# Performance work log

Hardware: AMD Instinct MI355X
Metric: run time of the kernel (lower is better)

Reference implementation:

```python
import jax, jax.numpy as jnp
from jax import lax
import numpy as np

B, S, D, H, O, V = 1024, 128, 256, 2048, 10, 10

def setup_inputs() -> dict:
    key = jax.random.key(0)
    ks = jax.random.split(key, 8)
    x = jax.random.randint(ks[0], (B, S), 0, V)
    embed = jax.random.normal(ks[1], (V, D), dtype=jnp.float32)
    sd_hx = 1.0 / np.sqrt(D)
    sd_hh = 1.0 / np.sqrt(H)
    W_hx = jax.random.uniform(ks[2], (H, D), minval=-sd_hx, maxval=sd_hx)
    b_hx = jax.random.uniform(ks[3], (H,), minval=-sd_hx, maxval=sd_hx)
    W_hh = jax.random.uniform(ks[4], (H, H), minval=-sd_hh, maxval=sd_hh)
    b_hh = jax.random.uniform(ks[5], (H,), minval=-sd_hh, maxval=sd_hh)
    W_oh = jax.random.uniform(ks[6], (O, H), minval=-sd_hh, maxval=sd_hh)
    b_oh = jax.random.uniform(ks[7], (O,), minval=-sd_hh, maxval=sd_hh)
    return {"x": x, "embed": embed, "W_hx": W_hx, "b_hx": b_hx,
            "W_hh": W_hh, "b_hh": b_hh, "W_oh": W_oh, "b_oh": b_oh}

def reference(x, embed, W_hx, b_hx, W_hh, b_hh, W_oh, b_oh):
    e = embed[x]                                   # [B,S,D]
    # precompute input-to-hidden projection for all steps (one big GEMM)
    xh = jnp.einsum('bsd,hd->bsh', e, W_hx) + b_hx  # [B,S,H]
    # step 0: torch code applies ONLY hx (no hh term, no hh bias)
    h0 = jnp.tanh(xh[:, 0])
    def step(h, xt):
        h = jnp.tanh(xt + h @ W_hh.T + b_hh)
        return h, None
    hT, _ = lax.scan(step, h0, jnp.swapaxes(xh[:, 1:], 0, 1))  # scan over time
    o = hT @ W_oh.T + b_oh                         # [B,O]
    return jax.nn.softmax(o, axis=1)               # nn.Softmax() on 2D -> dim=1
```

## Files before the change

kernel.cpp:

```cpp
#include <hip/hip_runtime.h>
#include <stdint.h>
#include <stddef.h>

#define B_ 1024
#define S_ 128
#define D_ 256
#define H_ 2048
#define O_ 10
#define V_ 10

#define BM 64
#define BN 64
#define BK 128
#define NKT (H_ / BK)

typedef unsigned short u16;
typedef short v8s __attribute__((ext_vector_type(8)));
typedef float v4f __attribute__((ext_vector_type(4)));
typedef u16 u16x4 __attribute__((ext_vector_type(4)));

__device__ __forceinline__ u16 f2bf(float f) {
  unsigned int u = __float_as_uint(f);
  u += 0x7FFFu + ((u >> 16) & 1u);
  return (u16)(u >> 16);
}
__device__ __forceinline__ float bf2f(u16 h) {
  return __uint_as_float(((unsigned int)h) << 16);
}
__device__ __forceinline__ float fast_tanh(float x) {
  float e = __expf(2.0f * x);
  return 1.0f - 2.0f / (e + 1.0f);
}
__device__ __forceinline__ void gl2lds16(const void* g, void* l) {
  __builtin_amdgcn_global_load_lds(
      (const __attribute__((address_space(1))) uint32_t*)g,
      (__attribute__((address_space(3))) uint32_t*)l, 16, 0, 0);
}

__global__ __launch_bounds__(256) void make_table(const float* __restrict__ embed,
                                                  const float* __restrict__ W_hx,
                                                  const float* __restrict__ b_hx,
                                                  float* __restrict__ Txh) {
  int idx = blockIdx.x * 256 + threadIdx.x;
  int v = idx >> 11, h = idx & 2047;
  const float4* e4 = (const float4*)(embed + v * D_);
  const float4* w4 = (const float4*)(W_hx + (size_t)h * D_);
  float s = b_hx[h];
#pragma unroll 4
  for (int d = 0; d < D_ / 4; ++d) {
    float4 a = e4[d], b = w4[d];
    s = fmaf(a.x, b.x, s); s = fmaf(a.y, b.y, s);
    s = fmaf(a.z, b.z, s); s = fmaf(a.w, b.w, s);
  }
  Txh[idx] = s;
}

__global__ __launch_bounds__(256) void conv_w(const float* __restrict__ W,
                                              u16* __restrict__ Wb) {
  int i = blockIdx.x * 256 + threadIdx.x;
  float4 w = ((const float4*)W)[i];
  u16x4 o = { f2bf(w.x), f2bf(w.y), f2bf(w.z), f2bf(w.w) };
  ((u16x4*)Wb)[i] = o;
}

__global__ __launch_bounds__(256) void init_h0(const float* __restrict__ Txh,
                                               const int* __restrict__ x,
                                               u16* __restrict__ H0) {
  int idx = blockIdx.x * 256 + threadIdx.x;
  int b = idx >> 11, j = idx & 2047;
  int xv = x[b * S_];
  H0[idx] = f2bf(fast_tanh(Txh[xv * H_ + j]));
}


__device__ __forceinline__ void stage_tiles(const u16* __restrict__ Hin,
                                            const u16* __restrict__ Wb,
                                            u16* __restrict__ As, u16* __restrict__ Bs,
                                            int bm, int bn, int kbase, int tid, int w) {
#pragma unroll
  for (int i = 0; i < 4; ++i) {
    int s = i * 256 + tid;
    int m = s >> 4;
    int cg = (s & 15) ^ (m & 15);
    const u16* g = Hin + (size_t)(bm + m) * H_ + kbase + cg * 8;
    u16* lp = As + (size_t)(i * 256 + (w << 6)) * 8;
    gl2lds16(g, lp);
  }
#pragma unroll
  for (int i = 0; i < 4; ++i) {
    int s = i * 256 + tid;
    int n = s >> 4;
    int cg = (s & 15) ^ (n & 15);
    const u16* g = Wb + (size_t)(bn + n) * H_ + kbase + cg * 8;
    u16* lp = Bs + (size_t)(i * 256 + (w << 6)) * 8;
    gl2lds16(g, lp);
  }
}

__global__ __launch_bounds__(256, 2) void rnn_step(const u16* __restrict__ Hin,
                                                   const u16* __restrict__ Wb,
                                                   const float* __restrict__ Txh,
                                                   const int* __restrict__ x,
                                                   const float* __restrict__ b_hh,
                                                   u16* __restrict__ Hout,
                                                   int t) {
  __shared__ __align__(16) u16 As[2][BM * BK];
  __shared__ __align__(16) u16 Bs[2][BN * BK];

  const int tid = threadIdx.x;
  const int bid = blockIdx.x;
  const int xcd = bid & 7;
  const int sl  = bid >> 3;
  const int xr = xcd >> 2, xc = xcd & 3;
  const int bm = (xr * 8 + (sl >> 3)) * BM;
  const int bn = (xc * 8 + (sl & 7)) * BN;

  const int w = tid >> 6, l = tid & 63;
  const int wr = w >> 1, wc = w & 1;
  const int lane16 = l & 15, quad = l >> 4;

  v4f acc[2][2];
#pragma unroll
  for (int i = 0; i < 2; ++i)
#pragma unroll
    for (int j = 0; j < 2; ++j) acc[i][j] = (v4f){0.f, 0.f, 0.f, 0.f};

  stage_tiles(Hin, Wb, As[0], Bs[0], bm, bn, 0, tid, w);
  __syncthreads();

  for (int kt = 0; kt < NKT; ++kt) {
    const int cur = kt & 1;
    if (kt + 1 < NKT)
      stage_tiles(Hin, Wb, As[cur ^ 1], Bs[cur ^ 1], bm, bn, (kt + 1) * BK, tid, w);

#pragma unroll
    for (int kc = 0; kc < 4; ++kc) {
      const int cc = kc * 4 + quad;
      v8s a[2], bf[2];
#pragma unroll
      for (int i = 0; i < 2; ++i) {
        int m = wr * 32 + i * 16 + lane16;
        a[i] = *(const v8s*)&As[cur][(m * 16 + (cc ^ lane16)) * 8];
      }
#pragma unroll
      for (int j = 0; j < 2; ++j) {
        int n = wc * 32 + j * 16 + lane16;
        bf[j] = *(const v8s*)&Bs[cur][(n * 16 + (cc ^ lane16)) * 8];
      }
#pragma unroll
      for (int i = 0; i < 2; ++i)
#pragma unroll
        for (int j = 0; j < 2; ++j)
          acc[i][j] = __builtin_amdgcn_mfma_f32_16x16x32_bf16(a[i], bf[j], acc[i][j], 0, 0, 0);
    }
    __syncthreads();
  }

  const int colb = bn + wc * 32 + lane16;
  float bh[2];
#pragma unroll
  for (int j = 0; j < 2; ++j) bh[j] = b_hh[colb + j * 16];
#pragma unroll
  for (int i = 0; i < 2; ++i) {
#pragma unroll
    for (int r = 0; r < 4; ++r) {
      int row = bm + wr * 32 + i * 16 + quad * 4 + r;
      const float* trow = Txh + x[row * S_ + t] * H_;
      u16* orow = Hout + (size_t)row * H_;
#pragma unroll
      for (int j = 0; j < 2; ++j) {
        int col = colb + j * 16;
        float v = acc[i][j][r] + trow[col] + bh[j];
        orow[col] = f2bf(fast_tanh(v));
      }
    }
  }
}

__global__ __launch_bounds__(256) void out_softmax(const u16* __restrict__ Hf,
                                                   const float* __restrict__ W_oh,
                                                   const float* __restrict__ b_oh,
                                                   float* __restrict__ out) {
  int b = blockIdx.x, tid = threadIdx.x;
  float hv[8];
  const u16* hr = Hf + (size_t)b * H_ + tid * 8;
#pragma unroll
  for (int u = 0; u < 8; ++u) hv[u] = bf2f(hr[u]);
  float acc[O_];
#pragma unroll
  for (int i = 0; i < O_; ++i) {
    const float* wr = W_oh + (size_t)i * H_ + tid * 8;
    float s = 0.f;
#pragma unroll
    for (int u = 0; u < 8; ++u) s = fmaf(hv[u], wr[u], s);
    acc[i] = s;
  }
#pragma unroll
  for (int off = 32; off > 0; off >>= 1)
#pragma unroll
    for (int i = 0; i < O_; ++i) acc[i] += __shfl_down(acc[i], off);
  __shared__ float red[4][O_];
  if ((tid & 63) == 0)
#pragma unroll
    for (int i = 0; i < O_; ++i) red[tid >> 6][i] = acc[i];
  __syncthreads();
  if (tid == 0) {
    float o[O_], mx = -1e30f;
#pragma unroll
    for (int i = 0; i < O_; ++i) {
      o[i] = red[0][i] + red[1][i] + red[2][i] + red[3][i] + b_oh[i];
      mx = fmaxf(mx, o[i]);
    }
    float se = 0.f;
#pragma unroll
    for (int i = 0; i < O_; ++i) { o[i] = __expf(o[i] - mx); se += o[i]; }
    float inv = 1.f / se;
#pragma unroll
    for (int i = 0; i < O_; ++i) out[b * O_ + i] = o[i] * inv;
  }
}

extern "C" void kernel_launch(void* const* d_in, const int* in_sizes, int n_in,
                              void* d_out, int out_size, void* d_ws, size_t ws_size,
                              hipStream_t stream) {
  const int*   x     = (const int*)  d_in[0];
  const float* embed = (const float*)d_in[1];
  const float* W_hx  = (const float*)d_in[2];
  const float* b_hx  = (const float*)d_in[3];
  const float* W_hh  = (const float*)d_in[4];
  const float* b_hh  = (const float*)d_in[5];
  const float* W_oh  = (const float*)d_in[6];
  const float* b_oh  = (const float*)d_in[7];
  float* out = (float*)d_out;

  char* ws = (char*)d_ws;
  float* Txh = (float*)ws;
  u16* Wb = (u16*)(ws + (80 << 10));
  u16* Ha = (u16*)(ws + (80 << 10) + (8 << 20));
  u16* Hb = (u16*)(ws + (80 << 10) + (12 << 20));

  make_table<<<80, 256, 0, stream>>>(embed, W_hx, b_hx, Txh);
  conv_w<<<4096, 256, 0, stream>>>(W_hh, Wb);
  init_h0<<<8192, 256, 0, stream>>>(Txh, x, Ha);

  for (int t = 1; t < S_; ++t) {
    const u16* hin = (t & 1) ? Ha : Hb;
    u16* hout = (t & 1) ? Hb : Ha;
    rnn_step<<<512, 256, 0, stream>>>(hin, Wb, Txh, x, b_hh, hout, t);
  }
  out_softmax<<<B_, 256, 0, stream>>>(Hb, W_oh, b_oh, out);
}
```

Measured before the change: 2.325 ms.

## Use 128x64 tiles with 512 threads and a three-stage LDS pipeline

Each recurrent-step block now computes a 128x64 output tile with 8 waves, halving the grid to 256 blocks. It keeps three LDS stages loaded through global_load_lds, governed by explicit vmcnt waits and raw barriers. All four k-chunks of fragments are read from LDS before the MFMAs are issued under a raised wave priority. The aim is to hide global-load latency and improve reuse of the weight tile, at the cost of 144KB of dynamic LDS, which limits each CU to one block.

```diff
diff --git a/kernel.cpp b/kernel.cpp
--- a/kernel.cpp
+++ b/kernel.cpp
@@ -9,10 +9,13 @@
 #define O_ 10
 #define V_ 10
 
-#define BM 64
+#define BM 128
 #define BN 64
 #define BK 128
 #define NKT (H_ / BK)
+#define NSTG 3
+#define STG_ELEMS ((BM + BN) * BK)
+#define SMEM_BYTES (NSTG * STG_ELEMS * 2)
 
 typedef unsigned short u16;
 typedef short v8s __attribute__((ext_vector_type(8)));
@@ -79,40 +82,39 @@
                                             int bm, int bn, int kbase, int tid, int w) {
 #pragma unroll
   for (int i = 0; i < 4; ++i) {
-    int s = i * 256 + tid;
+    int s = i * 512 + tid;
     int m = s >> 4;
     int cg = (s & 15) ^ (m & 15);
     const u16* g = Hin + (size_t)(bm + m) * H_ + kbase + cg * 8;
-    u16* lp = As + (size_t)(i * 256 + (w << 6)) * 8;
+    u16* lp = As + (size_t)(i * 512 + (w << 6)) * 8;
     gl2lds16(g, lp);
   }
 #pragma unroll
-  for (int i = 0; i < 4; ++i) {
-    int s = i * 256 + tid;
+  for (int i = 0; i < 2; ++i) {
+    int s = i * 512 + tid;
     int n = s >> 4;
     int cg = (s & 15) ^ (n & 15);
     const u16* g = Wb + (size_t)(bn + n) * H_ + kbase + cg * 8;
-    u16* lp = Bs + (size_t)(i * 256 + (w << 6)) * 8;
+    u16* lp = Bs + (size_t)(i * 512 + (w << 6)) * 8;
     gl2lds16(g, lp);
   }
 }
 
-__global__ __launch_bounds__(256, 2) void rnn_step(const u16* __restrict__ Hin,
+__global__ __launch_bounds__(512, 2) void rnn_step(const u16* __restrict__ Hin,
                                                    const u16* __restrict__ Wb,
                                                    const float* __restrict__ Txh,
                                                    const int* __restrict__ x,
                                                    const float* __restrict__ b_hh,
                                                    u16* __restrict__ Hout,
                                                    int t) {
-  __shared__ __align__(16) u16 As[2][BM * BK];
-  __shared__ __align__(16) u16 Bs[2][BN * BK];
+  extern __shared__ __align__(16) u16 smem[];
 
   const int tid = threadIdx.x;
   const int bid = blockIdx.x;
   const int xcd = bid & 7;
   const int sl  = bid >> 3;
   const int xr = xcd >> 2, xc = xcd & 3;
-  const int bm = (xr * 8 + (sl >> 3)) * BM;
+  const int bm = (xr * 4 + (sl >> 3)) * BM;
   const int bn = (xc * 8 + (sl & 7)) * BN;
 
   const int w = tid >> 6, l = tid & 63;
@@ -125,35 +127,57 @@
 #pragma unroll
     for (int j = 0; j < 2; ++j) acc[i][j] = (v4f){0.f, 0.f, 0.f, 0.f};
 
-  stage_tiles(Hin, Wb, As[0], Bs[0], bm, bn, 0, tid, w);
-  __syncthreads();
+  {
+    u16* s0 = smem;
+    u16* s1 = smem + STG_ELEMS;
+    stage_tiles(Hin, Wb, s0, s0 + BM * BK, bm, bn, 0, tid, w);
+    stage_tiles(Hin, Wb, s1, s1 + BM * BK, bm, bn, BK, tid, w);
+  }
 
   for (int kt = 0; kt < NKT; ++kt) {
-    const int cur = kt & 1;
-    if (kt + 1 < NKT)
-      stage_tiles(Hin, Wb, As[cur ^ 1], Bs[cur ^ 1], bm, bn, (kt + 1) * BK, tid, w);
-
+    __builtin_amdgcn_s_barrier();
+    asm volatile("" ::: "memory");
+
+    if (kt + 2 < NKT) {
+      u16* sb = smem + ((kt + 2) % 3) * STG_ELEMS;
+      stage_tiles(Hin, Wb, sb, sb + BM * BK, bm, bn, (kt + 2) * BK, tid, w);
+    }
+
+    if (kt < NKT - 2)       asm volatile("s_waitcnt vmcnt(12)" ::: "memory");
+    else if (kt == NKT - 2) asm volatile("s_waitcnt vmcnt(6)"  ::: "memory");
+    else                    asm volatile("s_waitcnt vmcnt(0)"  ::: "memory");
+
+    __builtin_amdgcn_s_barrier();
+    asm volatile("" ::: "memory");
+
+    const u16* Asb = smem + (kt % 3) * STG_ELEMS;
+    const u16* Bsb = Asb + BM * BK;
+
+    v8s af[4][2], bf[4][2];
 #pragma unroll
     for (int kc = 0; kc < 4; ++kc) {
       const int cc = kc * 4 + quad;
-      v8s a[2], bf[2];
 #pragma unroll
       for (int i = 0; i < 2; ++i) {
         int m = wr * 32 + i * 16 + lane16;
-        a[i] = *(const v8s*)&As[cur][(m * 16 + (cc ^ lane16)) * 8];
+        af[kc][i] = *(const v8s*)&Asb[(m * 16 + (cc ^ lane16)) * 8];
       }
 #pragma unroll
       for (int j = 0; j < 2; ++j) {
         int n = wc * 32 + j * 16 + lane16;
-        bf[j] = *(const v8s*)&Bs[cur][(n * 16 + (cc ^ lane16)) * 8];
+        bf[kc][j] = *(const v8s*)&Bsb[(n * 16 + (cc ^ lane16)) * 8];
       }
+    }
+    __builtin_amdgcn_s_setprio(1);
+#pragma unroll
+    for (int kc = 0; kc < 4; ++kc)
 #pragma unroll
       for (int i = 0; i < 2; ++i)
 #pragma unroll
         for (int j = 0; j < 2; ++j)
-          acc[i][j] = __builtin_amdgcn_mfma_f32_16x16x32_bf16(a[i], bf[j], acc[i][j], 0, 0, 0);
-    }
-    __syncthreads();
+          acc[i][j] = __builtin_amdgcn_mfma_f32_16x16x32_bf16(af[kc][i], bf[kc][j],
+                                                              acc[i][j], 0, 0, 0);
+    __builtin_amdgcn_s_setprio(0);
   }
 
   const int colb = bn + wc * 32 + lane16;
@@ -233,6 +257,13 @@
   const float* b_oh  = (const float*)d_in[7];
   float* out = (float*)d_out;
 
+  static bool attr_set = false;
+  if (!attr_set) {
+    (void)hipFuncSetAttribute(reinterpret_cast<const void*>(rnn_step),
+                              hipFuncAttributeMaxDynamicSharedMemorySize, SMEM_BYTES);
+    attr_set = true;
+  }
+
   char* ws = (char*)d_ws;
   float* Txh = (float*)ws;
   u16* Wb = (u16*)(ws + (80 << 10));
@@ -246,7 +277,7 @@
   for (int t = 1; t < S_; ++t) {
     const u16* hin = (t & 1) ? Ha : Hb;
     u16* hout = (t & 1) ? Hb : Ha;
-    rnn_step<<<512, 256, 0, stream>>>(hin, Wb, Txh, x, b_hh, hout, t);
+    rnn_step<<<256, 512, SMEM_BYTES, stream>>>(hin, Wb, Txh, x, b_hh, hout, t);
   }
   out_softmax<<<B_, 256, 0, stream>>>(Hb, W_oh, b_oh, out);
 }
```

New measurement: 2.275 ms. -2.2%, faster.
